# Kernel tuning notes

Measured on AMD Instinct MI355X. Metric: run time of the kernel, lower is better.

## Reference

```python
import jax, jax.numpy as jnp
import numpy as np

EMBED_DIM = 1024
Q_DIM = 512
KV_DIM = 512
NUM_HEADS = 16
HEAD_DIM = EMBED_DIM // NUM_HEADS
EPS = 1e-5


def setup_inputs() -> dict:
    key = jax.random.key(0)
    ks = jax.random.split(key, 13)
    B, N1, N2 = 2, 2048, 2048
    s_q = 1.0 / np.sqrt(Q_DIM)
    s_kv = 1.0 / np.sqrt(KV_DIM)
    s_e = 1.0 / np.sqrt(EMBED_DIM)
    return {
        "query": jax.random.normal(ks[0], (B, N1, Q_DIM), jnp.float32),
        "key": jax.random.normal(ks[1], (B, N2, KV_DIM), jnp.float32),
        "value": jax.random.normal(ks[2], (B, N2, KV_DIM), jnp.float32),
        "Wq": jax.random.uniform(ks[3], (Q_DIM, EMBED_DIM), jnp.float32, -s_q, s_q),
        "bq": jax.random.uniform(ks[4], (EMBED_DIM,), jnp.float32, -s_q, s_q),
        "Wk": jax.random.uniform(ks[5], (KV_DIM, EMBED_DIM), jnp.float32, -s_kv, s_kv),
        "bk": jax.random.uniform(ks[6], (EMBED_DIM,), jnp.float32, -s_kv, s_kv),
        "Wv": jax.random.uniform(ks[7], (KV_DIM, EMBED_DIM), jnp.float32, -s_kv, s_kv),
        "bv": jax.random.uniform(ks[8], (EMBED_DIM,), jnp.float32, -s_kv, s_kv),
        "Wo": jax.random.uniform(ks[9], (EMBED_DIM, EMBED_DIM), jnp.float32, -s_e, s_e),
        "bo": jax.random.uniform(ks[10], (EMBED_DIM,), jnp.float32, -s_e, s_e),
        "gamma": jnp.ones((EMBED_DIM,), jnp.float32),
        "beta": jnp.zeros((EMBED_DIM,), jnp.float32),
    }


def reference(query, key, value, Wq, bq, Wk, bk, Wv, bv, Wo, bo, gamma, beta):
    B, N1, _ = query.shape
    _, N2, _ = key.shape
    scale = HEAD_DIM ** (-0.5)
    # projections -> [B, H, N, D]
    Q = (query @ Wq + bq).reshape(B, N1, NUM_HEADS, HEAD_DIM).transpose(0, 2, 1, 3)
    K = (key @ Wk + bk).reshape(B, N2, NUM_HEADS, HEAD_DIM).transpose(0, 2, 1, 3)
    V = (value @ Wv + bv).reshape(B, N2, NUM_HEADS, HEAD_DIM).transpose(0, 2, 1, 3)
    # full score matrix [B, H, N1, N2] (matches original eager attention)
    att = jnp.einsum("bhqd,bhkd->bhqk", Q, K) * scale
    att = jax.nn.softmax(att, axis=-1)
    # dropout is identity in eval mode
    out = jnp.einsum("bhqk,bhkd->bhqd", att, V)  # [B, H, N1, D]
    out = out.transpose(0, 2, 1, 3).reshape(B, N1, EMBED_DIM)
    out = out @ Wo + bo
    # LayerNorm
    mu = out.mean(-1, keepdims=True)
    var = ((out - mu) ** 2).mean(-1, keepdims=True)
    return (out - mu) * jax.lax.rsqrt(var + EPS) * gamma + beta
```

## Files before the change

kernel.cpp:

```cpp
#include <hip/hip_runtime.h>

typedef __bf16 bf16x8 __attribute__((ext_vector_type(8)));
typedef __bf16 bf16x4 __attribute__((ext_vector_type(4)));
typedef float f32x4 __attribute__((ext_vector_type(4)));
typedef unsigned short u16;
typedef unsigned int u32;

__device__ __forceinline__ f32x4 mfma16(bf16x8 a, bf16x8 b, f32x4 c) {
  return __builtin_amdgcn_mfma_f32_16x16x32_bf16(a, b, c, 0, 0, 0);
}

__device__ __forceinline__ void gload_lds16(const void* g, void* l) {
  __builtin_amdgcn_global_load_lds(
      (const __attribute__((address_space(1))) void*)g,
      (__attribute__((address_space(3))) void*)l, 16, 0, 0);
}

__global__ __launch_bounds__(256) void tobf16_3(const float4* __restrict__ a,
                                                const float4* __restrict__ b,
                                                const float4* __restrict__ c,
                                                bf16x4* __restrict__ oa,
                                                bf16x4* __restrict__ ob,
                                                bf16x4* __restrict__ oc, int n4) {
  int i = blockIdx.x * 256 + threadIdx.x;
  if (i >= n4) return;
  const int z = blockIdx.y;
  const float4* in = z == 0 ? a : z == 1 ? b : c;
  bf16x4* out = z == 0 ? oa : z == 1 ? ob : oc;
  float4 v = in[i];
  bf16x4 o;
  o[0] = (__bf16)v.x; o[1] = (__bf16)v.y; o[2] = (__bf16)v.z; o[3] = (__bf16)v.w;
  out[i] = o;
}

__global__ __launch_bounds__(256) void wtrans4(const float* __restrict__ W0,
                                               const float* __restrict__ W1,
                                               const float* __restrict__ W2,
                                               const float* __restrict__ W3,
                                               u16* __restrict__ T0, u16* __restrict__ T1,
                                               u16* __restrict__ T2, u16* __restrict__ T3) {
  const int z = blockIdx.z;
  const int K = (z == 3) ? 1024 : 512;
  const int N = 1024;
  const int k0 = blockIdx.y * 32;
  if (k0 >= K) return;
  const float* W = z == 0 ? W0 : z == 1 ? W1 : z == 2 ? W2 : W3;
  u16* Wt = z == 0 ? T0 : z == 1 ? T1 : z == 2 ? T2 : T3;
  __shared__ float t[32][33];
  const int tx = threadIdx.x, ty = threadIdx.y;
  const int n0 = blockIdx.x * 32;
#pragma unroll
  for (int i = 0; i < 4; ++i)
    t[ty + i * 8][tx] = W[(size_t)(k0 + ty + i * 8) * N + n0 + tx];
  __syncthreads();
#pragma unroll
  for (int i = 0; i < 4; ++i)
    ((__bf16*)Wt)[(size_t)(n0 + ty + i * 8) * K + k0 + tx] = (__bf16)t[tx][ty + i * 8];
}

template <int MODE, int DBUF>
__device__ __forceinline__ void gemm_body(const u16* __restrict__ A,
                                          const u16* __restrict__ Bt,
                                          const float* __restrict__ bias,
                                          void* __restrict__ Cout,
                                          int M, int N, int K, float scl) {
  constexpr int NB = DBUF ? 2 : 1;
  __shared__ __align__(16) u16 lA[NB][128 * 64];
  __shared__ __align__(16) u16 lB[NB][128 * 64];
  const int tid = threadIdx.x;
  const int w = tid >> 6, l = tid & 63;
  const int li = l & 15, lg = l >> 4;
  const int wm = w & 1, wn = w >> 1;
  const int bm = blockIdx.x * 128, bn = blockIdx.y * 128;

  f32x4 acc[4][4] = {};
  const int nk = K >> 6;

  auto stage = [&](int kt, int bufi) {
    const int k0 = kt << 6;
#pragma unroll
    for (int i = 0; i < 4; ++i) {
      const int c0 = (i * 4 + w) * 64;
      const int f = c0 + l;
      const int r = f >> 3, cs = (f & 7) ^ (r & 7);
      gload_lds16(A + (size_t)(bm + r) * K + k0 + cs * 8, &lA[bufi][c0 * 8]);
      gload_lds16(Bt + (size_t)(bn + r) * K + k0 + cs * 8, &lB[bufi][c0 * 8]);
    }
  };

  int cur = 0;
  if (DBUF) {
    stage(0, 0);
    __syncthreads();
  }

  for (int kt = 0; kt < nk; ++kt) {
    if (DBUF) {
      if (kt + 1 < nk) stage(kt + 1, cur ^ 1);
    } else {
      stage(kt, 0);
      __syncthreads();
    }
    bf16x8 af[4][2], bfr[4][2];
#pragma unroll
    for (int m = 0; m < 4; ++m) {
      const int row = wm * 64 + m * 16 + li;
#pragma unroll
      for (int kk = 0; kk < 2; ++kk) {
        const int kc = (lg + kk * 4) ^ (row & 7);
        af[m][kk] = *(const bf16x8*)&lA[cur][row * 64 + kc * 8];
      }
    }
#pragma unroll
    for (int n = 0; n < 4; ++n) {
      const int row = wn * 64 + n * 16 + li;
#pragma unroll
      for (int kk = 0; kk < 2; ++kk) {
        const int kc = (lg + kk * 4) ^ (row & 7);
        bfr[n][kk] = *(const bf16x8*)&lB[cur][row * 64 + kc * 8];
      }
    }
#pragma unroll
    for (int m = 0; m < 4; ++m)
#pragma unroll
      for (int n = 0; n < 4; ++n) {
        acc[m][n] = mfma16(af[m][0], bfr[n][0], acc[m][n]);
        acc[m][n] = mfma16(af[m][1], bfr[n][1], acc[m][n]);
      }
    __syncthreads();
    if (DBUF) cur ^= 1;
  }

#pragma unroll
  for (int m = 0; m < 4; ++m) {
    const int row0 = bm + wm * 64 + m * 16 + lg * 4;
#pragma unroll
    for (int n = 0; n < 4; ++n) {
      const int col = bn + wn * 64 + n * 16 + li;
      const float bv = bias[col];
      if (MODE == 2) {
        const int bq = row0 >> 11, kv = row0 & 2047;
        bf16x4 pk;
#pragma unroll
        for (int r = 0; r < 4; ++r) pk[r] = (__bf16)((acc[m][n][r] + bv) * scl);
        *(bf16x4*)&((u16*)Cout)[((size_t)(bq * 1024 + col)) * 2048 + kv] = pk;
      } else {
#pragma unroll
        for (int r = 0; r < 4; ++r) {
          float v = (acc[m][n][r] + bv) * scl;
          ((__bf16*)Cout)[(size_t)(row0 + r) * N + col] = (__bf16)v;
        }
      }
    }
  }
}

__global__ __launch_bounds__(256) void gemm_qkv(const u16* __restrict__ xq,
                                                const u16* __restrict__ xk,
                                                const u16* __restrict__ xv,
                                                const u16* __restrict__ wqt,
                                                const u16* __restrict__ wkt,
                                                const u16* __restrict__ wvt,
                                                const float* __restrict__ bq,
                                                const float* __restrict__ bk,
                                                const float* __restrict__ bv,
                                                u16* __restrict__ Qb, u16* __restrict__ Kb,
                                                u16* __restrict__ Vt, float qscale) {
  const int z = blockIdx.z;
  if (z == 0) {
    gemm_body<0, 0>(xq, wqt, bq, Qb, 4096, 1024, 512, qscale);
  } else if (z == 1) {
    gemm_body<0, 0>(xk, wkt, bk, Kb, 4096, 1024, 512, 1.0f);
  } else {
    gemm_body<2, 0>(xv, wvt, bv, Vt, 4096, 1024, 512, 1.0f);
  }
}

__global__ __launch_bounds__(256) void gemm_o(const u16* __restrict__ A,
                                              const u16* __restrict__ Bt,
                                              const float* __restrict__ bias,
                                              u16* __restrict__ C) {
  gemm_body<0, 1>(A, Bt, bias, C, 4096, 1024, 1024, 1.0f);
}

__global__ __launch_bounds__(512) void attn64(const u16* __restrict__ Qb,
                                              const u16* __restrict__ Kb,
                                              const u16* __restrict__ Vt,
                                              u16* __restrict__ Ob,
                                              int N1, int N2) {
  const int tid = threadIdx.x;
  const int w = tid >> 6, l = tid & 63;
  const int li = l & 15, lg = l >> 4;

  const int flat = blockIdx.x + 8 * (blockIdx.y + 16 * blockIdx.z);
  const int xcd = flat & 7, idx = flat >> 3;
  const int qb = idx & 7, pr = idx >> 3;
  const int h = 2 * xcd + (pr & 1);
  const int b = pr >> 1;
  const int q0 = qb * 256;

  __shared__ __align__(16) u16 lK[2][64 * 64];
  __shared__ __align__(16) u16 lV[2][64 * 64];
  __shared__ __align__(16) u32 lP[8][2][16 * 32];

  bf16x8 qa[2][2];
#pragma unroll
  for (int s = 0; s < 2; ++s) {
    const size_t qoff = (size_t)(b * N1 + q0 + s * 128 + w * 16 + li) * 1024 + h * 64;
    qa[s][0] = *(const bf16x8*)&Qb[qoff + lg * 8];
    qa[s][1] = *(const bf16x8*)&Qb[qoff + 32 + lg * 8];
  }

  const u16* Kbase = Kb + (size_t)b * N2 * 1024 + h * 64;
  const u16* Vbase = Vt + (size_t)((b * 16 + h) * 64) * N2;

  const int sr = tid >> 3;
  const int sc = (tid & 7) ^ (sr & 7);

  f32x4 o[2][4] = {};
  float lsum0 = 0.f, lsum1 = 0.f;
  u32* lP0 = &lP[w][0][0];
  u32* lP1 = &lP[w][1][0];
  const int sw = (li & 7) << 2;
  const int ca = lg ^ (li & 7), cb = (lg + 4) ^ (li & 7);

  const int nt = N2 >> 6;
  int cur = 0;
  gload_lds16(Kbase + (size_t)sr * 1024 + sc * 8, &lK[0][w * 512]);
  gload_lds16(Vbase + (size_t)sr * N2 + sc * 8, &lV[0][w * 512]);
  __syncthreads();

  for (int t = 0; t < nt; ++t) {
    if (t + 1 < nt) {
      gload_lds16(Kbase + (size_t)((t + 1) * 64 + sr) * 1024 + sc * 8, &lK[cur ^ 1][w * 512]);
      gload_lds16(Vbase + (size_t)sr * N2 + (t + 1) * 64 + sc * 8, &lV[cur ^ 1][w * 512]);
    }
    const u16* K_ = lK[cur];
    const u16* V_ = lV[cur];

    float st0 = 0.f, st1 = 0.f;
    __builtin_amdgcn_s_setprio(1);
#pragma unroll
    for (int n = 0; n < 4; ++n) {
      const int row = n * 16 + li;
      bf16x8 k0 = *(const bf16x8*)&K_[row * 64 + ca * 8];
      bf16x8 k1 = *(const bf16x8*)&K_[row * 64 + cb * 8];
      f32x4 a = {}, a2 = {};
      a = mfma16(k0, qa[0][0], a);
      a = mfma16(k1, qa[0][1], a);
      a2 = mfma16(k0, qa[1][0], a2);
      a2 = mfma16(k1, qa[1][1], a2);
      float p0 = __builtin_amdgcn_exp2f(a[0]);
      float p1 = __builtin_amdgcn_exp2f(a[1]);
      float p2 = __builtin_amdgcn_exp2f(a[2]);
      float p3 = __builtin_amdgcn_exp2f(a[3]);
      st0 += (p0 + p1) + (p2 + p3);
      bf16x4 pk;
      pk[0] = (__bf16)p0; pk[1] = (__bf16)p1; pk[2] = (__bf16)p2; pk[3] = (__bf16)p3;
      *(bf16x4*)&lP0[li * 32 + ((n * 8 + lg * 2) ^ sw)] = pk;
      float q0p = __builtin_amdgcn_exp2f(a2[0]);
      float q1p = __builtin_amdgcn_exp2f(a2[1]);
      float q2p = __builtin_amdgcn_exp2f(a2[2]);
      float q3p = __builtin_amdgcn_exp2f(a2[3]);
      st1 += (q0p + q1p) + (q2p + q3p);
      bf16x4 pk2;
      pk2[0] = (__bf16)q0p; pk2[1] = (__bf16)q1p; pk2[2] = (__bf16)q2p; pk2[3] = (__bf16)q3p;
      *(bf16x4*)&lP1[li * 32 + ((n * 8 + lg * 2) ^ sw)] = pk2;
    }
    __builtin_amdgcn_s_setprio(0);
    lsum0 += st0;
    lsum1 += st1;

    __builtin_amdgcn_s_setprio(1);
#pragma unroll
    for (int ks = 0; ks < 2; ++ks) {
      const bf16x8 pf0 = *(const bf16x8*)&lP0[li * 32 + ((ks * 16 + lg * 4) ^ sw)];
      const bf16x8 pf1 = *(const bf16x8*)&lP1[li * 32 + ((ks * 16 + lg * 4) ^ sw)];
#pragma unroll
      for (int dt = 0; dt < 4; ++dt) {
        const int row = dt * 16 + li;
        const int c = (lg + ks * 4) ^ (li & 7);
        const bf16x8 vf = *(const bf16x8*)&V_[row * 64 + c * 8];
        o[0][dt] = mfma16(vf, pf0, o[0][dt]);
        o[1][dt] = mfma16(vf, pf1, o[1][dt]);
      }
    }
    __builtin_amdgcn_s_setprio(0);
    __syncthreads();
    cur ^= 1;
  }

  lsum0 += __shfl_xor(lsum0, 16, 64);
  lsum0 += __shfl_xor(lsum0, 32, 64);
  lsum1 += __shfl_xor(lsum1, 16, 64);
  lsum1 += __shfl_xor(lsum1, 32, 64);
  const float inv0 = 1.f / lsum0;
  const float inv1 = 1.f / lsum1;

#pragma unroll
  for (int s = 0; s < 2; ++s) {
    const float inv = s == 0 ? inv0 : inv1;
    const size_t orow = (size_t)(b * N1 + q0 + s * 128 + w * 16 + li) * 1024 + h * 64;
#pragma unroll
    for (int dt = 0; dt < 4; ++dt) {
      bf16x4 pk;
#pragma unroll
      for (int r = 0; r < 4; ++r) pk[r] = (__bf16)(o[s][dt][r] * inv);
      *(bf16x4*)&Ob[orow + dt * 16 + lg * 4] = pk;
    }
  }
}

__global__ __launch_bounds__(256) void lnorm(const u16* __restrict__ X,
                                             const float* __restrict__ gamma,
                                             const float* __restrict__ beta,
                                             float* __restrict__ out) {
  const int row = blockIdx.x;
  const int tid = threadIdx.x;
  const bf16x4 xv = ((const bf16x4*)(X + (size_t)row * 1024))[tid];
  float4 v;
  v.x = (float)xv[0]; v.y = (float)xv[1]; v.z = (float)xv[2]; v.w = (float)xv[3];
  float s = v.x + v.y + v.z + v.w;
  float sq = v.x * v.x + v.y * v.y + v.z * v.z + v.w * v.w;
#pragma unroll
  for (int d = 1; d < 64; d <<= 1) {
    s += __shfl_xor(s, d, 64);
    sq += __shfl_xor(sq, d, 64);
  }
  __shared__ float red[8];
  const int w = tid >> 6, l = tid & 63;
  if (l == 0) { red[w] = s; red[4 + w] = sq; }
  __syncthreads();
  s = red[0] + red[1] + red[2] + red[3];
  sq = red[4] + red[5] + red[6] + red[7];
  const float mu = s * (1.f / 1024.f);
  const float var = sq * (1.f / 1024.f) - mu * mu;
  const float rstd = rsqrtf(var + 1e-5f);
  const float4 g = ((const float4*)gamma)[tid];
  const float4 bb = ((const float4*)beta)[tid];
  float4 o;
  o.x = (v.x - mu) * rstd * g.x + bb.x;
  o.y = (v.y - mu) * rstd * g.y + bb.y;
  o.z = (v.z - mu) * rstd * g.z + bb.z;
  o.w = (v.w - mu) * rstd * g.w + bb.w;
  ((float4*)(out + (size_t)row * 1024))[tid] = o;
}

extern "C" void kernel_launch(void* const* d_in, const int* in_sizes, int n_in,
                              void* d_out, int out_size, void* d_ws, size_t ws_size,
                              hipStream_t stream) {
  const float* query = (const float*)d_in[0];
  const float* key_ = (const float*)d_in[1];
  const float* value = (const float*)d_in[2];
  const float* Wq = (const float*)d_in[3];
  const float* bq = (const float*)d_in[4];
  const float* Wk = (const float*)d_in[5];
  const float* bk = (const float*)d_in[6];
  const float* Wv = (const float*)d_in[7];
  const float* bv = (const float*)d_in[8];
  const float* Wo = (const float*)d_in[9];
  const float* bo = (const float*)d_in[10];
  const float* gamma = (const float*)d_in[11];
  const float* beta = (const float*)d_in[12];

  constexpr int B = 2, N1 = 2048, N2 = 2048, E = 1024, QKD = 512;
  constexpr int M = B * N1;
  const float QSCALE = 0.125f * 1.4426950408889634f;

  char* p = (char*)d_ws;
  auto alloc = [&](size_t bytes) {
    char* r = p;
    p += (bytes + 255) & ~(size_t)255;
    return r;
  };
  u16* xq = (u16*)alloc((size_t)M * QKD * 2);
  u16* xk = (u16*)alloc((size_t)M * QKD * 2);
  u16* xv = (u16*)alloc((size_t)M * QKD * 2);
  u16* wqt = (u16*)alloc((size_t)E * QKD * 2);
  u16* wkt = (u16*)alloc((size_t)E * QKD * 2);
  u16* wvt = (u16*)alloc((size_t)E * QKD * 2);
  u16* wot = (u16*)alloc((size_t)E * E * 2);
  u16* Qb = (u16*)alloc((size_t)M * E * 2);
  u16* Kb = (u16*)alloc((size_t)M * E * 2);
  u16* Vt = (u16*)alloc((size_t)M * E * 2);
  u16* ao = (u16*)alloc((size_t)M * E * 2);
  u16* ao2 = (u16*)alloc((size_t)M * E * 2);

  const int n4 = M * QKD / 4;
  tobf16_3<<<dim3((n4 + 255) / 256, 3), 256, 0, stream>>>(
      (const float4*)query, (const float4*)key_, (const float4*)value,
      (bf16x4*)xq, (bf16x4*)xk, (bf16x4*)xv, n4);

  wtrans4<<<dim3(E / 32, 32, 4), dim3(32, 8), 0, stream>>>(
      Wq, Wk, Wv, Wo, wqt, wkt, wvt, wot);

  gemm_qkv<<<dim3(M / 128, E / 128, 3), 256, 0, stream>>>(
      xq, xk, xv, wqt, wkt, wvt, bq, bk, bv, Qb, Kb, Vt, QSCALE);

  attn64<<<dim3(N1 / 256, 16, B), 512, 0, stream>>>(Qb, Kb, Vt, ao, N1, N2);

  gemm_o<<<dim3(M / 128, E / 128), 256, 0, stream>>>(ao, wot, bo, ao2);

  lnorm<<<M, 256, 0, stream>>>(ao2, gamma, beta, (float*)d_out);
}
```

Before: 113.5 us.

## Split attention KV range across two blocks and merge partials in a combine kernel

The attention kernel now processes half of the key/value sequence per block, doubling the grid. Each half writes unnormalized bf16 outputs and per-row softmax sums, and a new combine kernel adds the halves and normalizes them. The aim is more resident blocks per compute unit to hide latency, at the cost of extra partial-buffer traffic, an extra launch and bf16 rounding of the partials. The input bf16 cast and the weight transpose kernels are also merged into one prep launch to save a launch.

```diff
diff --git a/kernel.cpp b/kernel.cpp
--- a/kernel.cpp
+++ b/kernel.cpp
@@ -16,46 +16,48 @@
       (__attribute__((address_space(3))) void*)l, 16, 0, 0);
 }
 
-__global__ __launch_bounds__(256) void tobf16_3(const float4* __restrict__ a,
-                                                const float4* __restrict__ b,
-                                                const float4* __restrict__ c,
-                                                bf16x4* __restrict__ oa,
-                                                bf16x4* __restrict__ ob,
-                                                bf16x4* __restrict__ oc, int n4) {
-  int i = blockIdx.x * 256 + threadIdx.x;
-  if (i >= n4) return;
+__global__ __launch_bounds__(256) void prep(const float4* __restrict__ qi,
+                                            const float4* __restrict__ ki,
+                                            const float4* __restrict__ vi,
+                                            bf16x4* __restrict__ oq,
+                                            bf16x4* __restrict__ ok,
+                                            bf16x4* __restrict__ ov,
+                                            const float* __restrict__ W0,
+                                            const float* __restrict__ W1,
+                                            const float* __restrict__ W2,
+                                            const float* __restrict__ W3,
+                                            u16* __restrict__ T0, u16* __restrict__ T1,
+                                            u16* __restrict__ T2, u16* __restrict__ T3,
+                                            int n4) {
   const int z = blockIdx.y;
-  const float4* in = z == 0 ? a : z == 1 ? b : c;
-  bf16x4* out = z == 0 ? oa : z == 1 ? ob : oc;
-  float4 v = in[i];
-  bf16x4 o;
-  o[0] = (__bf16)v.x; o[1] = (__bf16)v.y; o[2] = (__bf16)v.z; o[3] = (__bf16)v.w;
-  out[i] = o;
-}
-
-__global__ __launch_bounds__(256) void wtrans4(const float* __restrict__ W0,
-                                               const float* __restrict__ W1,
-                                               const float* __restrict__ W2,
-                                               const float* __restrict__ W3,
-                                               u16* __restrict__ T0, u16* __restrict__ T1,
-                                               u16* __restrict__ T2, u16* __restrict__ T3) {
-  const int z = blockIdx.z;
-  const int K = (z == 3) ? 1024 : 512;
-  const int N = 1024;
-  const int k0 = blockIdx.y * 32;
-  if (k0 >= K) return;
-  const float* W = z == 0 ? W0 : z == 1 ? W1 : z == 2 ? W2 : W3;
-  u16* Wt = z == 0 ? T0 : z == 1 ? T1 : z == 2 ? T2 : T3;
-  __shared__ float t[32][33];
-  const int tx = threadIdx.x, ty = threadIdx.y;
-  const int n0 = blockIdx.x * 32;
-#pragma unroll
-  for (int i = 0; i < 4; ++i)
-    t[ty + i * 8][tx] = W[(size_t)(k0 + ty + i * 8) * N + n0 + tx];
-  __syncthreads();
-#pragma unroll
-  for (int i = 0; i < 4; ++i)
-    ((__bf16*)Wt)[(size_t)(n0 + ty + i * 8) * K + k0 + tx] = (__bf16)t[tx][ty + i * 8];
+  const int tid = threadIdx.x;
+  if (z < 3) {
+    int i = blockIdx.x * 256 + tid;
+    if (i >= n4) return;
+    const float4* in = z == 0 ? qi : z == 1 ? ki : vi;
+    bf16x4* out = z == 0 ? oq : z == 1 ? ok : ov;
+    float4 v = in[i];
+    bf16x4 o;
+    o[0] = (__bf16)v.x; o[1] = (__bf16)v.y; o[2] = (__bf16)v.z; o[3] = (__bf16)v.w;
+    out[i] = o;
+  } else {
+    const int zz = z - 3;
+    const int K = (zz == 3) ? 1024 : 512;
+    const int nb = (K / 32) * 32;
+    if (blockIdx.x >= nb) return;
+    const float* W = zz == 0 ? W0 : zz == 1 ? W1 : zz == 2 ? W2 : W3;
+    u16* Wt = zz == 0 ? T0 : zz == 1 ? T1 : zz == 2 ? T2 : T3;
+    __shared__ float t[32][33];
+    const int tx = tid & 31, ty = tid >> 5;
+    const int n0 = (blockIdx.x & 31) * 32, k0 = (blockIdx.x >> 5) * 32;
+#pragma unroll
+    for (int i = 0; i < 4; ++i)
+      t[ty + i * 8][tx] = W[(size_t)(k0 + ty + i * 8) * 1024 + n0 + tx];
+    __syncthreads();
+#pragma unroll
+    for (int i = 0; i < 4; ++i)
+      ((__bf16*)Wt)[(size_t)(n0 + ty + i * 8) * K + k0 + tx] = (__bf16)t[tx][ty + i * 8];
+  }
 }
 
 template <int MODE, int DBUF>
@@ -186,7 +188,8 @@
 __global__ __launch_bounds__(512) void attn64(const u16* __restrict__ Qb,
                                               const u16* __restrict__ Kb,
                                               const u16* __restrict__ Vt,
-                                              u16* __restrict__ Ob,
+                                              u16* __restrict__ Opart,
+                                              float* __restrict__ Lpart,
                                               int N1, int N2) {
   const int tid = threadIdx.x;
   const int w = tid >> 6, l = tid & 63;
@@ -194,9 +197,10 @@
 
   const int flat = blockIdx.x + 8 * (blockIdx.y + 16 * blockIdx.z);
   const int xcd = flat & 7, idx = flat >> 3;
-  const int qb = idx & 7, pr = idx >> 3;
-  const int h = 2 * xcd + (pr & 1);
-  const int b = pr >> 1;
+  const int qb = idx & 7, rest = idx >> 3;
+  const int h = 2 * xcd + (rest & 1);
+  const int b = (rest >> 1) & 1;
+  const int kvh = rest >> 2;
   const int q0 = qb * 256;
 
   __shared__ __align__(16) u16 lK[2][64 * 64];
@@ -224,14 +228,15 @@
   const int sw = (li & 7) << 2;
   const int ca = lg ^ (li & 7), cb = (lg + 4) ^ (li & 7);
 
-  const int nt = N2 >> 6;
+  const int t0 = kvh * 16;
   int cur = 0;
-  gload_lds16(Kbase + (size_t)sr * 1024 + sc * 8, &lK[0][w * 512]);
-  gload_lds16(Vbase + (size_t)sr * N2 + sc * 8, &lV[0][w * 512]);
+  gload_lds16(Kbase + (size_t)(t0 * 64 + sr) * 1024 + sc * 8, &lK[0][w * 512]);
+  gload_lds16(Vbase + (size_t)sr * N2 + t0 * 64 + sc * 8, &lV[0][w * 512]);
   __syncthreads();
 
-  for (int t = 0; t < nt; ++t) {
-    if (t + 1 < nt) {
+  for (int tt = 0; tt < 16; ++tt) {
+    const int t = t0 + tt;
+    if (tt + 1 < 16) {
       gload_lds16(Kbase + (size_t)((t + 1) * 64 + sr) * 1024 + sc * 8, &lK[cur ^ 1][w * 512]);
       gload_lds16(Vbase + (size_t)sr * N2 + (t + 1) * 64 + sc * 8, &lV[cur ^ 1][w * 512]);
     }
@@ -294,21 +299,39 @@
   lsum0 += __shfl_xor(lsum0, 32, 64);
   lsum1 += __shfl_xor(lsum1, 16, 64);
   lsum1 += __shfl_xor(lsum1, 32, 64);
-  const float inv0 = 1.f / lsum0;
-  const float inv1 = 1.f / lsum1;
-
+
+  u16* Op = Opart + (size_t)kvh * 4096 * 1024;
 #pragma unroll
   for (int s = 0; s < 2; ++s) {
-    const float inv = s == 0 ? inv0 : inv1;
-    const size_t orow = (size_t)(b * N1 + q0 + s * 128 + w * 16 + li) * 1024 + h * 64;
+    const int qrow = b * N1 + q0 + s * 128 + w * 16 + li;
+    const size_t orow = (size_t)qrow * 1024 + h * 64;
 #pragma unroll
     for (int dt = 0; dt < 4; ++dt) {
       bf16x4 pk;
 #pragma unroll
-      for (int r = 0; r < 4; ++r) pk[r] = (__bf16)(o[s][dt][r] * inv);
-      *(bf16x4*)&Ob[orow + dt * 16 + lg * 4] = pk;
-    }
-  }
+      for (int r = 0; r < 4; ++r) pk[r] = (__bf16)o[s][dt][r];
+      *(bf16x4*)&Op[orow + dt * 16 + lg * 4] = pk;
+    }
+    if (lg == 0)
+      Lpart[(size_t)kvh * 4096 * 16 + (size_t)qrow * 16 + h] = (s == 0 ? lsum0 : lsum1);
+  }
+}
+
+__global__ __launch_bounds__(256) void combine(const u16* __restrict__ Opart,
+                                               const float* __restrict__ Lpart,
+                                               u16* __restrict__ ao) {
+  const int row = blockIdx.x;
+  const int tid = threadIdx.x;
+  const int h = tid >> 4;
+  const float l = Lpart[(size_t)row * 16 + h] + Lpart[4096 * 16 + (size_t)row * 16 + h];
+  const float inv = 1.f / l;
+  const size_t off = (size_t)row * 1024 + tid * 4;
+  const bf16x4 a = *(const bf16x4*)&Opart[off];
+  const bf16x4 b = *(const bf16x4*)&Opart[(size_t)4096 * 1024 + off];
+  bf16x4 o;
+#pragma unroll
+  for (int j = 0; j < 4; ++j) o[j] = (__bf16)(((float)a[j] + (float)b[j]) * inv);
+  *(bf16x4*)&ao[off] = o;
 }
 
 __global__ __launch_bounds__(256) void lnorm(const u16* __restrict__ X,
@@ -385,19 +408,21 @@
   u16* Vt = (u16*)alloc((size_t)M * E * 2);
   u16* ao = (u16*)alloc((size_t)M * E * 2);
   u16* ao2 = (u16*)alloc((size_t)M * E * 2);
+  u16* Opart = (u16*)alloc((size_t)2 * M * E * 2);
+  float* Lpart = (float*)alloc((size_t)2 * M * 16 * 4);
 
   const int n4 = M * QKD / 4;
-  tobf16_3<<<dim3((n4 + 255) / 256, 3), 256, 0, stream>>>(
+  prep<<<dim3((n4 + 255) / 256, 7), 256, 0, stream>>>(
       (const float4*)query, (const float4*)key_, (const float4*)value,
-      (bf16x4*)xq, (bf16x4*)xk, (bf16x4*)xv, n4);
-
-  wtrans4<<<dim3(E / 32, 32, 4), dim3(32, 8), 0, stream>>>(
-      Wq, Wk, Wv, Wo, wqt, wkt, wvt, wot);
+      (bf16x4*)xq, (bf16x4*)xk, (bf16x4*)xv,
+      Wq, Wk, Wv, Wo, wqt, wkt, wvt, wot, n4);
 
   gemm_qkv<<<dim3(M / 128, E / 128, 3), 256, 0, stream>>>(
       xq, xk, xv, wqt, wkt, wvt, bq, bk, bv, Qb, Kb, Vt, QSCALE);
 
-  attn64<<<dim3(N1 / 256, 16, B), 512, 0, stream>>>(Qb, Kb, Vt, ao, N1, N2);
+  attn64<<<dim3(8, 16, 4), 512, 0, stream>>>(Qb, Kb, Vt, Opart, Lpart, N1, N2);
+
+  combine<<<M, 256, 0, stream>>>(Opart, Lpart, ao);
 
   gemm_o<<<dim3(M / 128, E / 128), 256, 0, stream>>>(ao, wot, bo, ao2);
 
```

Result: faster. 110.5 us (-2.7%).
